# Kernel tuning notes

Measured on AMD Instinct MI355X. Metric: run time of the kernel, lower is better.

## Reference

```python
import jax, jax.numpy as jnp
import numpy as np

ROPE_THETA = 10000.0


def _rotate_half(x):
    # interleaved rotation: out[..., 2i] = -x[..., 2i+1], out[..., 2i+1] = x[..., 2i]
    x_even = x[..., ::2]
    x_odd = x[..., 1::2]
    return jnp.stack([-x_odd, x_even], axis=-1).reshape(x.shape)


def _rope_cos_sin(N, D, dtype):
    inv_freq = 1.0 / (ROPE_THETA ** (jnp.arange(0, D, 2, dtype=jnp.float32) / D))  # [D/2]
    angles = jnp.arange(N, dtype=jnp.float32)[:, None] * inv_freq[None, :]          # [N, D/2]
    angles = jnp.repeat(angles, 2, axis=-1)                                          # [N, D]
    cos = jnp.cos(angles).astype(dtype)[None, :, None, :]  # [1, N, 1, D]
    sin = jnp.sin(angles).astype(dtype)[None, :, None, :]
    return cos, sin


def setup_inputs() -> dict:
    key = jax.random.key(0)
    kq, kk, kv, km = jax.random.split(key, 4)
    B, N, H, D = 16, 1024, 8, 64
    xq = jax.random.normal(kq, (B, N, H, D), dtype=jnp.float32)
    xk = jax.random.normal(kk, (B, N, H, D), dtype=jnp.float32)
    xv = jax.random.normal(kv, (B, N, H, D), dtype=jnp.float32)
    vis_mask = jax.random.bernoulli(km, 0.8, (B, N))  # bool visibility mask per batch
    return {"xq": xq, "xk": xk, "xv": xv, "vis_mask": vis_mask}


def reference(xq, xk, xv, vis_mask):
    B, N, H, D = xq.shape
    sm_scale = 1.0 / np.sqrt(D).astype(np.float32)

    # RoPE (interleaved) on q and k
    cos, sin = _rope_cos_sin(N, D, xq.dtype)
    q = xq * cos + _rotate_half(xq) * sin
    k = xk * cos + _rotate_half(xk) * sin

    # masked full attention: scores [B, H, N, N]
    scores = jnp.einsum("bnhd,bmhd->bhnm", q, k) * sm_scale
    attn_mask = (vis_mask[:, None, :, None] & vis_mask[:, None, None, :])  # [B,1,N,N]
    scores = jnp.where(attn_mask, scores, -jnp.inf)
    p = jax.nn.softmax(scores, axis=-1)
    p = jnp.nan_to_num(p, nan=0.0)  # fully-masked rows -> zeros (matches fallback)
    out = jnp.einsum("bhnm,bmhd->bnhd", p, xv)
    return out
```

## Files before the change

kernel.cpp:

```cpp
#include <hip/hip_runtime.h>
#include <hip/hip_bf16.h>
#include <stdint.h>

#define Bb 16
#define Nn 1024
#define Hh 8
#define Dd 64

typedef unsigned short u16;
typedef float f32x4 __attribute__((ext_vector_type(4)));
typedef short short8 __attribute__((ext_vector_type(8)));

union U4S8 { uint4 u; short8 s; };
union BF2U { __hip_bfloat162 h; uint32_t u; };

__device__ __forceinline__ uint32_t f2bf(float f){
  union{float f;uint32_t i;} v; v.f=f;
  return (v.i + 0x7fffu + ((v.i>>16)&1u))>>16;
}

__device__ __forceinline__ f32x4 mfma16(short8 a, short8 b, f32x4 c){
  return __builtin_amdgcn_mfma_f32_16x16x32_bf16(a,b,c,0,0,0);
}

#define ROPE_K 0.41524101186092030f
#define QS 0.18033688011112042f
#define NEGBIG -1.0e30f

__global__ __launch_bounds__(256) void rope_table_kernel(float2* __restrict__ tab)
{
  int id = blockIdx.x*256 + threadIdx.x;
  int n = id >> 5, i = id & 31;
  float inv = exp2f(-(float)i * ROPE_K);
  float sn, cs; sincosf((float)n * inv, &sn, &cs);
  tab[id] = make_float2(cs, sn);
}

struct Stage {
  float4 ka0, ka1, c0, c1;
  float v[8];
};

__device__ __forceinline__ void stage_load(Stage& S,
    const float* __restrict__ xk, const float* __restrict__ xv,
    const float2* __restrict__ tab, int b, int h, int n, int sd0,
    int vrow0, int vlane)
{
  const float4* kg = (const float4*)(xk + ((((size_t)b*Nn + n)*Hh + h)<<6) + sd0);
  S.ka0 = kg[0]; S.ka1 = kg[1];
  const float4* tg = (const float4*)(tab + (n<<5) + (sd0>>1));
  S.c0 = tg[0]; S.c1 = tg[1];
  const float* vb = xv + ((((size_t)b*Nn + vrow0)*Hh + h)<<6) + vlane;
  #pragma unroll
  for (int m=0;m<4;++m){
    S.v[2*m]   = vb[(16*m)*Hh*Dd];
    S.v[2*m+1] = vb[(16*m+1)*Hh*Dd];
  }
}

__device__ __forceinline__ void stage_write(const Stage& S,
    u16* __restrict__ Kl, u16* __restrict__ Vl, int kdest, int vdest)
{
  float kx[8]  = {S.ka0.x,S.ka0.y,S.ka0.z,S.ka0.w, S.ka1.x,S.ka1.y,S.ka1.z,S.ka1.w};
  float cs4[4] = {S.c0.x, S.c0.z, S.c1.x, S.c1.z};
  float sn4[4] = {S.c0.y, S.c0.w, S.c1.y, S.c1.w};
  uint32_t w[4];
  #pragma unroll
  for (int j=0;j<4;++j){
    float x0 = kx[2*j], x1 = kx[2*j+1];
    float q0 = x0*cs4[j] - x1*sn4[j];
    float q1 = x1*cs4[j] + x0*sn4[j];
    w[j] = f2bf(q0) | (f2bf(q1)<<16);
  }
  *(uint4*)&Kl[kdest] = make_uint4(w[0],w[1],w[2],w[3]);
  uint32_t wv[4];
  #pragma unroll
  for (int j=0;j<4;++j)
    wv[j] = f2bf(S.v[2*j]) | (f2bf(S.v[2*j+1])<<16);
  *(uint4*)&Vl[vdest] = make_uint4(wv[0],wv[1],wv[2],wv[3]);
}

__global__ __launch_bounds__(512,4) void fused_attn_kernel(
    const float* __restrict__ xq, const float* __restrict__ xk,
    const float* __restrict__ xv, const int* __restrict__ vis,
    const float2* __restrict__ tab, float* __restrict__ out)
{
  __shared__ u16 KV[2][2][4096];
  __shared__ float biasS[Nn];

  const int tid  = threadIdx.x;
  const int lane = tid & 63;
  const int wave = tid >> 6;
  const int l15  = lane & 15;
  const int quad = lane >> 4;

  const int bid = blockIdx.x;
  const int xcd = bid & 7;
  const int ix  = bid >> 3;
  const int bh_ = (xcd<<4) | (ix>>2);
  const int qt  = ix & 3;
  const int h   = bh_ & 7;
  const int b   = bh_ >> 3;
  const int qbase = qt<<8;

  const int* visb = vis + b*Nn;

  const int srow = ((tid>>6)<<3) | (tid & 7);
  const int sd0  = ((tid>>3) & 7) << 3;
  const int kdest = ((srow>>4)<<10) + ((sd0>>5)<<9) + (((sd0>>3)&3)<<7) + ((srow&15)<<3);
  const int vgrp  = tid >> 6;
  const int vlane = tid & 63;
  const int vdest = ((vlane>>4)<<10) + ((vgrp&1)<<9) + (((vgrp>>1)&3)<<7) + ((vlane&15)<<3);

  {
    int2 vi = *(const int2*)&visb[tid<<1];
    float2 bs;
    bs.x = vi.x ? 0.f : NEGBIG;
    bs.y = vi.y ? 0.f : NEGBIG;
    *(float2*)&biasS[tid<<1] = bs;
  }

  short8 qa[2][2];
  #pragma unroll
  for (int mb=0; mb<2; ++mb){
    int n = qbase + (wave<<5) + (mb<<4) + l15;
    const float* src = xq + ((((size_t)b*Nn + n)*Hh + h)<<6);
    #pragma unroll
    for (int half=0; half<2; ++half){
      int d0 = (half<<5) + (quad<<3);
      const float4* g = (const float4*)(src + d0);
      float4 u0 = g[0], u1 = g[1];
      float xx[8] = {u0.x,u0.y,u0.z,u0.w, u1.x,u1.y,u1.z,u1.w};
      uint32_t w[4];
      #pragma unroll
      for (int j=0;j<4;++j){
        int i2 = (d0>>1) + j;
        float2 t = tab[(n<<5)+i2];
        float x0 = xx[2*j], x1 = xx[2*j+1];
        float q0 = (x0*t.x - x1*t.y)*QS;
        float q1 = (x1*t.x + x0*t.y)*QS;
        w[j] = f2bf(q0) | (f2bf(q1)<<16);
      }
      U4S8 t2; t2.u = make_uint4(w[0],w[1],w[2],w[3]);
      qa[mb][half] = t2.s;
    }
  }

  U4S8 ones_u; ones_u.u = make_uint4(0x3F803F80u,0x3F803F80u,0x3F803F80u,0x3F803F80u);
  const short8 ones = ones_u.s;

  f32x4 acc[2][4];
  f32x4 l_acc[2];
  #pragma unroll
  for (int mb=0;mb<2;++mb){
    l_acc[mb] = (f32x4){0.f,0.f,0.f,0.f};
    #pragma unroll
    for (int s=0;s<4;++s) acc[mb][s] = (f32x4){0.f,0.f,0.f,0.f};
  }

  Stage S;
  stage_load(S, xk, xv, tab, b, h, srow, sd0, vgrp<<1, vlane);
  stage_write(S, &KV[0][0][0], &KV[0][1][0], kdest, vdest);
  stage_load(S, xk, xv, tab, b, h, 64 + srow, sd0, 64 + (vgrp<<1), vlane);
  __syncthreads();

  for (int kt=0; kt<16; ++kt){
    const int cur = kt & 1;

    uint32_t pk[4][2][2];
    __builtin_amdgcn_s_setprio(1);
    #pragma unroll
    for (int kb=0;kb<4;++kb){
      short8 kf0 = *(const short8*)&KV[cur][0][(kb<<10) + (lane<<3)];
      short8 kf1 = *(const short8*)&KV[cur][0][(kb<<10) + 512 + (lane<<3)];
      f32x4 bias = *(const f32x4*)&biasS[(kt<<6)+(kb<<4)+(quad<<2)];
      #pragma unroll
      for (int mb=0;mb<2;++mb){
        f32x4 t = mfma16(kf0, qa[mb][0], bias);
        t = mfma16(kf1, qa[mb][1], t);
        float p0 = __builtin_amdgcn_exp2f(t.x);
        float p1 = __builtin_amdgcn_exp2f(t.y);
        float p2 = __builtin_amdgcn_exp2f(t.z);
        float p3 = __builtin_amdgcn_exp2f(t.w);
        BF2U e0; e0.h = __float22bfloat162_rn(make_float2(p0,p1));
        BF2U e1; e1.h = __float22bfloat162_rn(make_float2(p2,p3));
        pk[kb][0][mb] = e0.u;
        pk[kb][1][mb] = e1.u;
      }
    }
    __builtin_amdgcn_s_setprio(0);

    short8 pa[2][2];
    #pragma unroll
    for (int mb=0;mb<2;++mb){
      U4S8 a0; a0.u = make_uint4(pk[0][0][mb], pk[1][0][mb], pk[2][0][mb], pk[3][0][mb]);
      U4S8 a1; a1.u = make_uint4(pk[0][1][mb], pk[1][1][mb], pk[2][1][mb], pk[3][1][mb]);
      pa[mb][0] = a0.s; pa[mb][1] = a1.s;
    }

    __builtin_amdgcn_s_setprio(1);
    #pragma unroll
    for (int mb=0;mb<2;++mb){
      l_acc[mb] = mfma16(pa[mb][0], ones, l_acc[mb]);
      l_acc[mb] = mfma16(pa[mb][1], ones, l_acc[mb]);
    }
    #pragma unroll
    for (int s=0;s<4;++s){
      short8 vb0 = *(const short8*)&KV[cur][1][(s<<10) + (lane<<3)];
      short8 vb1 = *(const short8*)&KV[cur][1][(s<<10) + 512 + (lane<<3)];
      #pragma unroll
      for (int mb=0;mb<2;++mb){
        acc[mb][s] = mfma16(pa[mb][0], vb0, acc[mb][s]);
        acc[mb][s] = mfma16(pa[mb][1], vb1, acc[mb][s]);
      }
    }
    __builtin_amdgcn_s_setprio(0);

    if (kt < 15)
      stage_write(S, &KV[cur^1][0][0], &KV[cur^1][1][0], kdest, vdest);
    if (kt < 14)
      stage_load(S, xk, xv, tab, b, h, ((kt+2)<<6) + srow, sd0,
                 ((kt+2)<<6) + (vgrp<<1), vlane);

    __syncthreads();
  }

  #pragma unroll
  for (int mb=0;mb<2;++mb){
    #pragma unroll
    for (int rr=0;rr<4;++rr){
      int qrow = qbase + (wave<<5) + (mb<<4) + (quad<<2) + rr;
      float lq = l_acc[mb][rr];
      float invl = (biasS[qrow] == 0.f && lq > 0.f) ? 1.f/lq : 0.f;
      float* ob = out + ((((size_t)b*Nn + qrow)*Hh + h)<<6);
      #pragma unroll
      for (int s=0;s<4;++s)
        ob[(s<<4)+l15] = acc[mb][s][rr]*invl;
    }
  }
}

__device__ __forceinline__ void stage_rope_row_fb(const float* __restrict__ src,
                                                  u16 (*dst)[72],
                                                  int n_global, int sr, int d0)
{
  const float4* g = (const float4*)src;
  float4 a0 = g[0], a1 = g[1], a2 = g[2], a3 = g[3];
  float xx[16] = {a0.x,a0.y,a0.z,a0.w, a1.x,a1.y,a1.z,a1.w,
                  a2.x,a2.y,a2.z,a2.w, a3.x,a3.y,a3.z,a3.w};
  uint32_t w[8];
  #pragma unroll
  for (int j=0;j<8;++j){
    int i = (d0>>1)+j;
    float inv = exp2f(-(float)i * ROPE_K);
    float ang = (float)n_global * inv;
    float sn, cs; sincosf(ang, &sn, &cs);
    float x0 = xx[2*j], x1 = xx[2*j+1];
    float q0 = x0*cs - x1*sn;
    float q1 = x1*cs + x0*sn;
    w[j] = f2bf(q0) | (f2bf(q1)<<16);
  }
  *(uint4*)&dst[sr][d0]   = make_uint4(w[0],w[1],w[2],w[3]);
  *(uint4*)&dst[sr][d0+8] = make_uint4(w[4],w[5],w[6],w[7]);
}

__global__ __launch_bounds__(256,2) void attn_fallback(
    const float* __restrict__ xq, const float* __restrict__ xk,
    const float* __restrict__ xv, const int* __restrict__ vis,
    float* __restrict__ out)
{
  __shared__ u16 Qs[64][72];
  __shared__ u16 Ks[64][72];
  __shared__ u16 Vt[64][72];
  __shared__ u16 Ps[4][16][72];
  __shared__ float viss[64];

  const int tid  = threadIdx.x;
  const int wave = tid >> 6;
  const int lane = tid & 63;
  const int l15  = lane & 15;
  const int quad = lane >> 4;

  const int bid = blockIdx.x;
  const int qt = bid & 15;
  const int h  = (bid >> 4) & 7;
  const int b  = bid >> 7;

  const int sr = tid >> 2;
  const int d0 = (tid & 3) << 4;

  {
    int ng = (qt<<6) + sr;
    const float* src = xq + ((((size_t)b*Nn + ng)*Hh + h)<<6) + d0;
    stage_rope_row_fb(src, Qs, ng, sr, d0);
  }
  __syncthreads();

  short8 qa0 = *(const short8*)&Qs[(wave<<4)+l15][quad<<3];
  short8 qa1 = *(const short8*)&Qs[(wave<<4)+l15][(quad<<3)+32];

  f32x4 acc[4];
  #pragma unroll
  for (int s=0;s<4;++s) acc[s] = (f32x4){0.f,0.f,0.f,0.f};
  float m_r[4], l_r[4];
  #pragma unroll
  for (int rr=0;rr<4;++rr){ m_r[rr] = -1e30f; l_r[rr] = 0.f; }

  for (int kt=0; kt<16; ++kt){
    __syncthreads();
    {
      int ng = (kt<<6) + sr;
      const float* src = xk + ((((size_t)b*Nn + ng)*Hh + h)<<6) + d0;
      stage_rope_row_fb(src, Ks, ng, sr, d0);
    }
    {
      int ng = (kt<<6) + sr;
      const float4* g = (const float4*)(xv + ((((size_t)b*Nn + ng)*Hh + h)<<6) + d0);
      float4 a0 = g[0], a1 = g[1], a2 = g[2], a3 = g[3];
      float vv16[16] = {a0.x,a0.y,a0.z,a0.w, a1.x,a1.y,a1.z,a1.w,
                        a2.x,a2.y,a2.z,a2.w, a3.x,a3.y,a3.z,a3.w};
      #pragma unroll
      for (int j=0;j<16;++j) Vt[d0+j][sr] = (u16)f2bf(vv16[j]);
    }
    if (tid < 64) viss[tid] = (vis[b*Nn + (kt<<6) + tid] != 0) ? 1.f : 0.f;
    __syncthreads();

    f32x4 s4[4];
    #pragma unroll
    for (int n=0;n<4;++n){
      short8 kb0 = *(const short8*)&Ks[(n<<4)+l15][quad<<3];
      short8 kb1 = *(const short8*)&Ks[(n<<4)+l15][(quad<<3)+32];
      f32x4 t = (f32x4){0.f,0.f,0.f,0.f};
      t = mfma16(qa0, kb0, t);
      t = mfma16(qa1, kb1, t);
      s4[n] = t;
    }
    float vv[4];
    #pragma unroll
    for (int n=0;n<4;++n) vv[n] = viss[(n<<4)+l15];

    float p[4][4];
    #pragma unroll
    for (int rr=0; rr<4; ++rr){
      float sc[4];
      #pragma unroll
      for (int n=0;n<4;++n) sc[n] = (vv[n] > 0.f) ? s4[n][rr]*0.125f : -1e30f;
      float tm = fmaxf(fmaxf(sc[0],sc[1]), fmaxf(sc[2],sc[3]));
      tm = fmaxf(tm, __shfl_xor(tm,1));
      tm = fmaxf(tm, __shfl_xor(tm,2));
      tm = fmaxf(tm, __shfl_xor(tm,4));
      tm = fmaxf(tm, __shfl_xor(tm,8));
      float mnew  = fmaxf(m_r[rr], tm);
      float alpha = __expf(m_r[rr] - mnew);
      m_r[rr] = mnew;
      float psum = 0.f;
      #pragma unroll
      for (int n=0;n<4;++n){
        float pv = (vv[n] > 0.f) ? __expf(sc[n] - mnew) : 0.f;
        p[n][rr] = pv; psum += pv;
      }
      l_r[rr] = l_r[rr]*alpha + psum;
      #pragma unroll
      for (int s=0;s<4;++s) acc[s][rr] *= alpha;
    }

    #pragma unroll
    for (int n=0;n<4;++n)
      #pragma unroll
      for (int rr=0;rr<4;++rr)
        Ps[wave][(quad<<2)+rr][(n<<4)+l15] = (u16)f2bf(p[n][rr]);
    asm volatile("s_waitcnt lgkmcnt(0)" ::: "memory");
    short8 pa0 = *(const short8*)&Ps[wave][l15][quad<<3];
    short8 pa1 = *(const short8*)&Ps[wave][l15][(quad<<3)+32];

    #pragma unroll
    for (int s=0;s<4;++s){
      short8 vb0 = *(const short8*)&Vt[(s<<4)+l15][quad<<3];
      short8 vb1 = *(const short8*)&Vt[(s<<4)+l15][(quad<<3)+32];
      acc[s] = mfma16(pa0, vb0, acc[s]);
      acc[s] = mfma16(pa1, vb1, acc[s]);
    }
  }

  #pragma unroll
  for (int rr=0;rr<4;++rr){
    float t = l_r[rr];
    t += __shfl_xor(t,1); t += __shfl_xor(t,2);
    t += __shfl_xor(t,4); t += __shfl_xor(t,8);
    int row = (qt<<6) + (wave<<4) + (quad<<2) + rr;
    int qv  = vis[b*Nn + row];
    float invl = (qv != 0 && t > 0.f) ? 1.f/t : 0.f;
    size_t obase = (((size_t)b*Nn + row)*Hh + h) << 6;
    #pragma unroll
    for (int s=0;s<4;++s)
      out[obase + (s<<4) + l15] = acc[s][rr]*invl;
  }
}

extern "C" void kernel_launch(void* const* d_in, const int* in_sizes, int n_in,
                              void* d_out, int out_size, void* d_ws, size_t ws_size,
                              hipStream_t stream)
{
  const float* xq = (const float*)d_in[0];
  const float* xk = (const float*)d_in[1];
  const float* xv = (const float*)d_in[2];
  const int* vis  = (const int*)d_in[3];
  float* out = (float*)d_out;

  const size_t tab_bytes = (size_t)32*1024*sizeof(float2);

  if (d_ws != nullptr && ws_size >= tab_bytes){
    float2* tab = (float2*)d_ws;
    rope_table_kernel<<<dim3(128), dim3(256), 0, stream>>>(tab);
    fused_attn_kernel<<<dim3(Bb*Hh*4), dim3(512), 0, stream>>>(xq, xk, xv, vis, tab, out);
  } else {
    attn_fallback<<<dim3(Bb*Hh*(Nn/64)), dim3(256), 0, stream>>>(xq, xk, xv, vis, out);
  }
}
```

Before: 178.7 us.

## Deepen K/V pipeline to four LDS stages and halve barriers per tile

```diff
diff --git a/kernel.cpp b/kernel.cpp
--- a/kernel.cpp
+++ b/kernel.cpp
@@ -14,9 +14,9 @@
 union U4S8 { uint4 u; short8 s; };
 union BF2U { __hip_bfloat162 h; uint32_t u; };
 
-__device__ __forceinline__ uint32_t f2bf(float f){
-  union{float f;uint32_t i;} v; v.f=f;
-  return (v.i + 0x7fffu + ((v.i>>16)&1u))>>16;
+__device__ __forceinline__ uint32_t packbf2(float lo, float hi){
+  BF2U t; t.h = __float22bfloat162_rn(make_float2(lo, hi));
+  return t.u;
 }
 
 __device__ __forceinline__ f32x4 mfma16(short8 a, short8 b, f32x4 c){
@@ -68,16 +68,68 @@
   #pragma unroll
   for (int j=0;j<4;++j){
     float x0 = kx[2*j], x1 = kx[2*j+1];
-    float q0 = x0*cs4[j] - x1*sn4[j];
-    float q1 = x1*cs4[j] + x0*sn4[j];
-    w[j] = f2bf(q0) | (f2bf(q1)<<16);
+    w[j] = packbf2(x0*cs4[j] - x1*sn4[j], x1*cs4[j] + x0*sn4[j]);
   }
   *(uint4*)&Kl[kdest] = make_uint4(w[0],w[1],w[2],w[3]);
   uint32_t wv[4];
   #pragma unroll
   for (int j=0;j<4;++j)
-    wv[j] = f2bf(S.v[2*j]) | (f2bf(S.v[2*j+1])<<16);
+    wv[j] = packbf2(S.v[2*j], S.v[2*j+1]);
   *(uint4*)&Vl[vdest] = make_uint4(wv[0],wv[1],wv[2],wv[3]);
+}
+
+__device__ __forceinline__ void compute_tile(
+    const u16* __restrict__ Kl, const u16* __restrict__ Vl,
+    const float* __restrict__ biasS, int kt, int lane, int quad,
+    const short8 (&qa)[2][2], short8 ones,
+    f32x4 (&acc)[2][4], f32x4 (&l_acc)[2])
+{
+  uint32_t pk[4][2][2];
+  __builtin_amdgcn_s_setprio(1);
+  #pragma unroll
+  for (int kb=0;kb<4;++kb){
+    short8 kf0 = *(const short8*)&Kl[(kb<<10) + (lane<<3)];
+    short8 kf1 = *(const short8*)&Kl[(kb<<10) + 512 + (lane<<3)];
+    f32x4 bias = *(const f32x4*)&biasS[(kt<<6)+(kb<<4)+(quad<<2)];
+    #pragma unroll
+    for (int mb=0;mb<2;++mb){
+      f32x4 t = mfma16(kf0, qa[mb][0], bias);
+      t = mfma16(kf1, qa[mb][1], t);
+      float p0 = __builtin_amdgcn_exp2f(t.x);
+      float p1 = __builtin_amdgcn_exp2f(t.y);
+      float p2 = __builtin_amdgcn_exp2f(t.z);
+      float p3 = __builtin_amdgcn_exp2f(t.w);
+      pk[kb][0][mb] = packbf2(p0,p1);
+      pk[kb][1][mb] = packbf2(p2,p3);
+    }
+  }
+  __builtin_amdgcn_s_setprio(0);
+
+  short8 pa[2][2];
+  #pragma unroll
+  for (int mb=0;mb<2;++mb){
+    U4S8 a0; a0.u = make_uint4(pk[0][0][mb], pk[1][0][mb], pk[2][0][mb], pk[3][0][mb]);
+    U4S8 a1; a1.u = make_uint4(pk[0][1][mb], pk[1][1][mb], pk[2][1][mb], pk[3][1][mb]);
+    pa[mb][0] = a0.s; pa[mb][1] = a1.s;
+  }
+
+  __builtin_amdgcn_s_setprio(1);
+  #pragma unroll
+  for (int mb=0;mb<2;++mb){
+    l_acc[mb] = mfma16(pa[mb][0], ones, l_acc[mb]);
+    l_acc[mb] = mfma16(pa[mb][1], ones, l_acc[mb]);
+  }
+  #pragma unroll
+  for (int s=0;s<4;++s){
+    short8 vb0 = *(const short8*)&Vl[(s<<10) + (lane<<3)];
+    short8 vb1 = *(const short8*)&Vl[(s<<10) + 512 + (lane<<3)];
+    #pragma unroll
+    for (int mb=0;mb<2;++mb){
+      acc[mb][s] = mfma16(pa[mb][0], vb0, acc[mb][s]);
+      acc[mb][s] = mfma16(pa[mb][1], vb1, acc[mb][s]);
+    }
+  }
+  __builtin_amdgcn_s_setprio(0);
 }
 
 __global__ __launch_bounds__(512,4) void fused_attn_kernel(
@@ -85,7 +137,7 @@
     const float* __restrict__ xv, const int* __restrict__ vis,
     const float2* __restrict__ tab, float* __restrict__ out)
 {
-  __shared__ u16 KV[2][2][4096];
+  __shared__ u16 KV[4][2][4096];
   __shared__ float biasS[Nn];
 
   const int tid  = threadIdx.x;
@@ -137,9 +189,7 @@
         int i2 = (d0>>1) + j;
         float2 t = tab[(n<<5)+i2];
         float x0 = xx[2*j], x1 = xx[2*j+1];
-        float q0 = (x0*t.x - x1*t.y)*QS;
-        float q1 = (x1*t.x + x0*t.y)*QS;
-        w[j] = f2bf(q0) | (f2bf(q1)<<16);
+        w[j] = packbf2((x0*t.x - x1*t.y)*QS, (x1*t.x + x0*t.y)*QS);
       }
       U4S8 t2; t2.u = make_uint4(w[0],w[1],w[2],w[3]);
       qa[mb][half] = t2.s;
@@ -158,70 +208,34 @@
     for (int s=0;s<4;++s) acc[mb][s] = (f32x4){0.f,0.f,0.f,0.f};
   }
 
-  Stage S;
-  stage_load(S, xk, xv, tab, b, h, srow, sd0, vgrp<<1, vlane);
-  stage_write(S, &KV[0][0][0], &KV[0][1][0], kdest, vdest);
-  stage_load(S, xk, xv, tab, b, h, 64 + srow, sd0, 64 + (vgrp<<1), vlane);
+  Stage S0, S1;
+  stage_load(S0, xk, xv, tab, b, h, srow, sd0, vgrp<<1, vlane);
+  stage_write(S0, &KV[0][0][0], &KV[0][1][0], kdest, vdest);
+  stage_load(S1, xk, xv, tab, b, h, 64 + srow, sd0, 64 + (vgrp<<1), vlane);
+  stage_write(S1, &KV[1][0][0], &KV[1][1][0], kdest, vdest);
+  stage_load(S0, xk, xv, tab, b, h, 128 + srow, sd0, 128 + (vgrp<<1), vlane);
+  stage_load(S1, xk, xv, tab, b, h, 192 + srow, sd0, 192 + (vgrp<<1), vlane);
   __syncthreads();
 
-  for (int kt=0; kt<16; ++kt){
-    const int cur = kt & 1;
-
-    uint32_t pk[4][2][2];
-    __builtin_amdgcn_s_setprio(1);
-    #pragma unroll
-    for (int kb=0;kb<4;++kb){
-      short8 kf0 = *(const short8*)&KV[cur][0][(kb<<10) + (lane<<3)];
-      short8 kf1 = *(const short8*)&KV[cur][0][(kb<<10) + 512 + (lane<<3)];
-      f32x4 bias = *(const f32x4*)&biasS[(kt<<6)+(kb<<4)+(quad<<2)];
-      #pragma unroll
-      for (int mb=0;mb<2;++mb){
-        f32x4 t = mfma16(kf0, qa[mb][0], bias);
-        t = mfma16(kf1, qa[mb][1], t);
-        float p0 = __builtin_amdgcn_exp2f(t.x);
-        float p1 = __builtin_amdgcn_exp2f(t.y);
-        float p2 = __builtin_amdgcn_exp2f(t.z);
-        float p3 = __builtin_amdgcn_exp2f(t.w);
-        BF2U e0; e0.h = __float22bfloat162_rn(make_float2(p0,p1));
-        BF2U e1; e1.h = __float22bfloat162_rn(make_float2(p2,p3));
-        pk[kb][0][mb] = e0.u;
-        pk[kb][1][mb] = e1.u;
-      }
-    }
-    __builtin_amdgcn_s_setprio(0);
-
-    short8 pa[2][2];
-    #pragma unroll
-    for (int mb=0;mb<2;++mb){
-      U4S8 a0; a0.u = make_uint4(pk[0][0][mb], pk[1][0][mb], pk[2][0][mb], pk[3][0][mb]);
-      U4S8 a1; a1.u = make_uint4(pk[0][1][mb], pk[1][1][mb], pk[2][1][mb], pk[3][1][mb]);
-      pa[mb][0] = a0.s; pa[mb][1] = a1.s;
-    }
-
-    __builtin_amdgcn_s_setprio(1);
-    #pragma unroll
-    for (int mb=0;mb<2;++mb){
-      l_acc[mb] = mfma16(pa[mb][0], ones, l_acc[mb]);
-      l_acc[mb] = mfma16(pa[mb][1], ones, l_acc[mb]);
-    }
-    #pragma unroll
-    for (int s=0;s<4;++s){
-      short8 vb0 = *(const short8*)&KV[cur][1][(s<<10) + (lane<<3)];
-      short8 vb1 = *(const short8*)&KV[cur][1][(s<<10) + 512 + (lane<<3)];
-      #pragma unroll
-      for (int mb=0;mb<2;++mb){
-        acc[mb][s] = mfma16(pa[mb][0], vb0, acc[mb][s]);
-        acc[mb][s] = mfma16(pa[mb][1], vb1, acc[mb][s]);
-      }
-    }
-    __builtin_amdgcn_s_setprio(0);
-
-    if (kt < 15)
-      stage_write(S, &KV[cur^1][0][0], &KV[cur^1][1][0], kdest, vdest);
-    if (kt < 14)
-      stage_load(S, xk, xv, tab, b, h, ((kt+2)<<6) + srow, sd0,
-                 ((kt+2)<<6) + (vgrp<<1), vlane);
-
+  for (int t=0; t<8; ++t){
+    const int k0 = 2*t, k1 = 2*t+1;
+
+    compute_tile(&KV[k0&3][0][0], &KV[k0&3][1][0], biasS, k0,
+                 lane, quad, qa, ones, acc, l_acc);
+    if (t < 7)
+      stage_write(S0, &KV[(k0+2)&3][0][0], &KV[(k0+2)&3][1][0], kdest, vdest);
+
+    compute_tile(&KV[k1&3][0][0], &KV[k1&3][1][0], biasS, k1,
+                 lane, quad, qa, ones, acc, l_acc);
+    if (t < 7)
+      stage_write(S1, &KV[(k1+2)&3][0][0], &KV[(k1+2)&3][1][0], kdest, vdest);
+
+    if (t < 6){
+      stage_load(S0, xk, xv, tab, b, h, ((k0+4)<<6) + srow, sd0,
+                 ((k0+4)<<6) + (vgrp<<1), vlane);
+      stage_load(S1, xk, xv, tab, b, h, ((k1+4)<<6) + srow, sd0,
+                 ((k1+4)<<6) + (vgrp<<1), vlane);
+    }
     __syncthreads();
   }
 
@@ -238,6 +252,11 @@
         ob[(s<<4)+l15] = acc[mb][s][rr]*invl;
     }
   }
+}
+
+__device__ __forceinline__ uint32_t f2bf(float f){
+  union{float f;uint32_t i;} v; v.f=f;
+  return (v.i + 0x7fffu + ((v.i>>16)&1u))>>16;
 }
 
 __device__ __forceinline__ void stage_rope_row_fb(const float* __restrict__ src,
```

After: 293.5 us. 1.64x slower.
